# Optimization experiments

Measured on AMD Instinct MI355X. Metric: run time of the kernel, lower is better.

The kernel has to match this reference:

```python
import jax, jax.numpy as jnp
import numpy as np

B, T, C, V = 8, 2048, 1024, 32000


def setup_inputs() -> dict:
    key = jax.random.key(0)
    ks = jax.random.split(key, 12)
    s = 1.0 / np.sqrt(C)
    return {
        "input_tokens": jax.random.randint(ks[0], (B, T), 0, V),
        "xx_init": jnp.zeros((B, C), jnp.float32),
        "aa_init": jnp.zeros((B, C), jnp.float32),
        "bb_init": jnp.zeros((B, C), jnp.float32),
        "pp_init": jnp.zeros((B, C), jnp.float32),  # with aa=bb=0 this is equivalent to -inf init
        "emb": jax.random.normal(ks[1], (V, C), jnp.float32) * 0.02,
        "time_mix_k": jax.random.uniform(ks[2], (C,), jnp.float32),
        "time_mix_v": jax.random.uniform(ks[3], (C,), jnp.float32),
        "time_mix_r": jax.random.uniform(ks[4], (C,), jnp.float32),
        "time_decay": jax.random.normal(ks[5], (C,), jnp.float32) * 0.1,
        "time_first": jax.random.normal(ks[6], (C,), jnp.float32) * 0.1,
        "Wk": jax.random.normal(ks[7], (C, C), jnp.float32) * s,
        "Wv": jax.random.normal(ks[8], (C, C), jnp.float32) * s,
        "Wr": jax.random.normal(ks[9], (C, C), jnp.float32) * s,
        "Wo": jax.random.normal(ks[10], (C, C), jnp.float32) * s,
    }


def _wkv_scan(k, v, aa0, bb0, pp0, w, u):
    """Numerically-stable RWKV WKV recurrence.
    k, v: [T, B, C]; aa0/bb0/pp0: [B, C]; w (decay, negative), u (bonus): [C]."""
    def step(carry, kv):
        aa, bb, pp = carry
        kt, vt = kv
        ww = u + kt
        p = jnp.maximum(pp, ww)
        e1 = jnp.exp(pp - p)
        e2 = jnp.exp(ww - p)
        wkv = (e1 * aa + e2 * vt) / (e1 * bb + e2)
        ww2 = pp + w
        p2 = jnp.maximum(ww2, kt)
        e1b = jnp.exp(ww2 - p2)
        e2b = jnp.exp(kt - p2)
        return (e1b * aa + e2b * vt, e1b * bb + e2b, p2), wkv
    (aa, bb, pp), out = jax.lax.scan(step, (aa0, bb0, pp0), (k, v))
    return out, aa, bb, pp


def _forward(input_tokens, xx_init, aa_init, bb_init, pp_init, emb,
             time_mix_k, time_mix_v, time_mix_r, time_decay, time_first,
             Wk, Wv, Wr, Wo):
    x = emb[input_tokens]                                   # [B, T, C]
    xprev = jnp.concatenate([xx_init[:, None, :], x[:, :-1]], axis=1)  # token shift
    xk = x * time_mix_k + xprev * (1.0 - time_mix_k)
    xv = x * time_mix_v + xprev * (1.0 - time_mix_v)
    xr = x * time_mix_r + xprev * (1.0 - time_mix_r)
    k = jnp.einsum("btc,dc->btd", xk, Wk)
    v = jnp.einsum("btc,dc->btd", xv, Wv)
    r = jax.nn.sigmoid(jnp.einsum("btc,dc->btd", xr, Wr))
    w = -jnp.exp(time_decay)                                # per-channel decay
    u = time_first
    wkv, _, _, _ = _wkv_scan(jnp.swapaxes(k, 0, 1), jnp.swapaxes(v, 0, 1),
                             aa_init, bb_init, pp_init, w, u)
    wkv = jnp.swapaxes(wkv, 0, 1)                           # [B, T, C]
    rwkv = jnp.einsum("btc,dc->btd", r * wkv, Wo)
    e1 = rwkv[:, -1]          # final-step state
    e2 = rwkv.mean(axis=1)    # time-averaged state
    hx = (e1 + e2) * 0.5
    return jnp.stack([hx, hx])  # (hx, cx) stacked -> [2, B, C]


def reference(input_tokens, xx_init, aa_init, bb_init, pp_init, emb,
              time_mix_k, time_mix_v, time_mix_r, time_decay, time_first,
              Wk, Wv, Wr, Wo):
    return _forward(input_tokens, xx_init, aa_init, bb_init, pp_init, emb,
                    time_mix_k, time_mix_v, time_mix_r, time_decay, time_first,
                    Wk, Wv, Wr, Wo)
```

## Files before the change

### kernel.cpp

```cpp
#include <hip/hip_runtime.h>

#define Bdim 8
#define Tdim 2048
#define Cdim 1024
#define CHUNK 128
#define NCHUNK 16
#define BC (Bdim*Cdim)

typedef float floatx4 __attribute__((ext_vector_type(4)));
typedef _Float16 half8 __attribute__((ext_vector_type(8)));
typedef _Float16 half4v __attribute__((ext_vector_type(4)));

__device__ __forceinline__ void load16(const void* g, void* l) {
    __builtin_amdgcn_global_load_lds(
        (const __attribute__((address_space(1))) void*)g,
        (__attribute__((address_space(3))) void*)l, 16, 0, 0);
}

__global__ __launch_bounds__(256) void embed_mix(const int* __restrict__ tokens,
                                                 const float* __restrict__ xx_init,
                                                 const float* __restrict__ emb,
                                                 _Float16* __restrict__ xe) {
    int row = blockIdx.x;
    int b = row / (Tdim + 1);
    int tt = row % (Tdim + 1);
    const float* src;
    if (tt == 0) src = xx_init + (size_t)b * Cdim;
    else         src = emb + (size_t)tokens[b * Tdim + tt - 1] * Cdim;
    int c0 = threadIdx.x * 4;
    float4 f = *reinterpret_cast<const float4*>(src + c0);
    half4v h;
    h[0] = (_Float16)f.x; h[1] = (_Float16)f.y; h[2] = (_Float16)f.z; h[3] = (_Float16)f.w;
    *reinterpret_cast<half4v*>(xe + (size_t)row * Cdim + c0) = h;
}

__global__ __launch_bounds__(256) void mix3(const _Float16* __restrict__ xe,
                                            const float* __restrict__ tmk,
                                            const float* __restrict__ tmv,
                                            const float* __restrict__ tmr,
                                            _Float16* __restrict__ xk,
                                            _Float16* __restrict__ xv,
                                            _Float16* __restrict__ xr) {
    int row = blockIdx.x;
    int b = row >> 11;
    int t = row & (Tdim - 1);
    const _Float16* cur = xe + ((size_t)(b * (Tdim + 1) + t + 1)) * Cdim;
    const _Float16* prv = cur - Cdim;
    int c = threadIdx.x * 4;
    half4v cu = *reinterpret_cast<const half4v*>(cur + c);
    half4v pv = *reinterpret_cast<const half4v*>(prv + c);
    float4 mk = *reinterpret_cast<const float4*>(tmk + c);
    float4 mv = *reinterpret_cast<const float4*>(tmv + c);
    float4 mr = *reinterpret_cast<const float4*>(tmr + c);
    half4v hk, hv, hr;
    float cf[4] = {(float)cu[0], (float)cu[1], (float)cu[2], (float)cu[3]};
    float pf[4] = {(float)pv[0], (float)pv[1], (float)pv[2], (float)pv[3]};
    float mkf[4] = {mk.x, mk.y, mk.z, mk.w};
    float mvf[4] = {mv.x, mv.y, mv.z, mv.w};
    float mrf[4] = {mr.x, mr.y, mr.z, mr.w};
    #pragma unroll
    for (int j = 0; j < 4; j++) {
        hk[j] = (_Float16)(mkf[j] * cf[j] + (1.0f - mkf[j]) * pf[j]);
        hv[j] = (_Float16)(mvf[j] * cf[j] + (1.0f - mvf[j]) * pf[j]);
        hr[j] = (_Float16)(mrf[j] * cf[j] + (1.0f - mrf[j]) * pf[j]);
    }
    size_t o = (size_t)row * Cdim + c;
    *reinterpret_cast<half4v*>(xk + o) = hk;
    *reinterpret_cast<half4v*>(xv + o) = hv;
    *reinterpret_cast<half4v*>(xr + o) = hr;
}

__global__ __launch_bounds__(256) void wconv(const float* __restrict__ Wk,
                                             const float* __restrict__ Wv,
                                             const float* __restrict__ Wr,
                                             _Float16* __restrict__ Wh) {
    const float* W = blockIdx.y == 0 ? Wk : (blockIdx.y == 1 ? Wv : Wr);
    _Float16* dst = Wh + (size_t)blockIdx.y * Cdim * Cdim;
    int i = (blockIdx.x * 256 + threadIdx.x) * 4;
    float4 f = *reinterpret_cast<const float4*>(W + i);
    half4v h;
    h[0] = (_Float16)f.x; h[1] = (_Float16)f.y; h[2] = (_Float16)f.z; h[3] = (_Float16)f.w;
    *reinterpret_cast<half4v*>(dst + i) = h;
}

__global__ __launch_bounds__(512, 2) void gemm_kvr(const _Float16* __restrict__ xk,
                                                   const _Float16* __restrict__ xv,
                                                   const _Float16* __restrict__ xr,
                                                   const _Float16* __restrict__ Wh,
                                                   _Float16* __restrict__ ko,
                                                   _Float16* __restrict__ vo,
                                                   _Float16* __restrict__ ro) {
    const int which = blockIdx.y;
    const _Float16* X = which == 0 ? xk : (which == 1 ? xv : xr);
    const _Float16* W = Wh + (size_t)which * Cdim * Cdim;
    _Float16* out     = which == 0 ? ko : (which == 1 ? vo : ro);

    const int lin = blockIdx.x;
    const int xcd = lin & 7;
    const int loc = lin >> 3;
    const int mt = xcd * 8 + (loc >> 2);
    const int nt = loc & 3;
    const int m0 = mt * 256;
    const int n0 = nt * 256;

    __shared__ _Float16 As[4 * 8192];
    __shared__ _Float16 Bs[4 * 8192];

    const int tid = threadIdx.x;
    const int lane = tid & 63;
    const int wave = tid >> 6;
    const int wm = (wave >> 2) * 128;
    const int wn = (wave & 3) * 64;
    const int lr = lane & 15;
    const int lk = lane >> 4;
    const int sw = (lr >> 1) & 3;

    const _Float16* Asrc = X + (size_t)m0 * Cdim;
    const _Float16* Bsrc = W + (size_t)n0 * Cdim;

    floatx4 acc[8][4] = {};

    auto stage = [&](int kt) {
        const int p = kt & 3;
        const int k0 = kt * 32;
        #pragma unroll
        for (int i = 0; i < 2; i++) {
            int e = i * 512 + tid;
            int r = e >> 2;
            int cp = e & 3;
            int cl = cp ^ ((r >> 1) & 3);
            load16(Asrc + (size_t)r * Cdim + k0 + cl * 8, (char*)(As + p * 8192) + e * 16);
        }
        #pragma unroll
        for (int i = 0; i < 2; i++) {
            int e = i * 512 + tid;
            int r = e >> 2;
            int cp = e & 3;
            int cl = cp ^ ((r >> 1) & 3);
            load16(Bsrc + (size_t)r * Cdim + k0 + cl * 8, (char*)(Bs + p * 8192) + e * 16);
        }
    };

    auto compute = [&](int kt) {
        const int p = kt & 3;
        const _Float16* ap = As + p * 8192 + (wm + lr) * 32 + (lk ^ sw) * 8;
        const _Float16* bp = Bs + p * 8192 + (wn + lr) * 32 + (lk ^ sw) * 8;
        half8 af[8], bf[4];
        #pragma unroll
        for (int mi = 0; mi < 8; mi++)
            af[mi] = *reinterpret_cast<const half8*>(ap + mi * 16 * 32);
        #pragma unroll
        for (int ni = 0; ni < 4; ni++)
            bf[ni] = *reinterpret_cast<const half8*>(bp + ni * 16 * 32);
        __builtin_amdgcn_s_setprio(1);
        #pragma unroll
        for (int mi = 0; mi < 8; mi++)
            #pragma unroll
            for (int ni = 0; ni < 4; ni++)
                acc[mi][ni] = __builtin_amdgcn_mfma_f32_16x16x32_f16(af[mi], bf[ni], acc[mi][ni], 0, 0, 0);
        __builtin_amdgcn_s_setprio(0);
    };

    stage(0); stage(1); stage(2);
    asm volatile("s_waitcnt vmcnt(8)" ::: "memory");
    __builtin_amdgcn_s_barrier();

    for (int kt = 0; kt < 29; ++kt) {
        stage(kt + 3);
        compute(kt);
        asm volatile("s_waitcnt vmcnt(8)" ::: "memory");
        __builtin_amdgcn_s_barrier();
    }
    compute(29);
    asm volatile("s_waitcnt vmcnt(4)" ::: "memory");
    __builtin_amdgcn_s_barrier();
    compute(30);
    asm volatile("s_waitcnt vmcnt(0)" ::: "memory");
    __builtin_amdgcn_s_barrier();
    compute(31);

    #pragma unroll
    for (int mi = 0; mi < 8; mi++) {
        #pragma unroll
        for (int ni = 0; ni < 4; ni++) {
            #pragma unroll
            for (int reg = 0; reg < 4; reg++) {
                int mm = m0 + wm + mi * 16 + (lane >> 4) * 4 + reg;
                int nn = n0 + wn + ni * 16 + (lane & 15);
                float v = acc[mi][ni][reg];
                if (which == 2) v = 1.0f / (1.0f + __expf(-v));
                out[(size_t)mm * Cdim + nn] = (_Float16)v;
            }
        }
    }
}

__global__ __launch_bounds__(256) void scan_pass1(const _Float16* __restrict__ kb,
                                                  const _Float16* __restrict__ vb,
                                                  const float* __restrict__ tdecay,
                                                  float* __restrict__ tot_a,
                                                  float* __restrict__ tot_b,
                                                  float* __restrict__ tot_p) {
    int idx = blockIdx.x * 256 + threadIdx.x;
    int j = idx >> 13;
    int bc = idx & (BC - 1);
    int b = bc >> 10;
    int c = bc & (Cdim - 1);
    float w = -__expf(tdecay[c]);
    float aa = 0.0f, bb = 0.0f, pp = -1e30f;
    const _Float16* kp = kb + ((size_t)(b * Tdim + j * CHUNK)) * Cdim + c;
    const _Float16* vp = vb + ((size_t)(b * Tdim + j * CHUNK)) * Cdim + c;
    #pragma unroll 4
    for (int t = 0; t < CHUNK; t++) {
        float kt = (float)kp[(size_t)t * Cdim];
        float vt = (float)vp[(size_t)t * Cdim];
        float ww2 = pp + w;
        float p2 = fmaxf(ww2, kt);
        float e1 = __expf(ww2 - p2);
        float e2 = __expf(kt - p2);
        aa = e1 * aa + e2 * vt;
        bb = e1 * bb + e2;
        pp = p2;
    }
    tot_a[idx] = aa; tot_b[idx] = bb; tot_p[idx] = pp;
}

__global__ __launch_bounds__(256) void combine_chunks(const float* __restrict__ tot_a,
                                                      const float* __restrict__ tot_b,
                                                      const float* __restrict__ tot_p,
                                                      const float* __restrict__ aa_init,
                                                      const float* __restrict__ bb_init,
                                                      const float* __restrict__ pp_init,
                                                      const float* __restrict__ tdecay,
                                                      float* __restrict__ inc_a,
                                                      float* __restrict__ inc_b,
                                                      float* __restrict__ inc_p) {
    int idx = blockIdx.x * 256 + threadIdx.x;
    int c = idx & (Cdim - 1);
    float w = -__expf(tdecay[c]);
    float wL = w * (float)CHUNK;
    float a = aa_init[idx], b = bb_init[idx], p = pp_init[idx];
    for (int j = 0; j < NCHUNK; j++) {
        inc_a[j * BC + idx] = a;
        inc_b[j * BC + idx] = b;
        inc_p[j * BC + idx] = p;
        float ta = tot_a[j * BC + idx];
        float tb = tot_b[j * BC + idx];
        float tp = tot_p[j * BC + idx];
        float px = p + wL;
        float q = fmaxf(px, tp);
        float e1 = __expf(px - q);
        float e2 = __expf(tp - q);
        a = e1 * a + e2 * ta;
        b = e1 * b + e2 * tb;
        p = q;
    }
}

__global__ __launch_bounds__(256) void scan_pass2(const _Float16* __restrict__ kb,
                                                  const _Float16* __restrict__ vb,
                                                  const _Float16* __restrict__ rb,
                                                  const float* __restrict__ tdecay,
                                                  const float* __restrict__ tfirst,
                                                  const float* __restrict__ inc_a,
                                                  const float* __restrict__ inc_b,
                                                  const float* __restrict__ inc_p,
                                                  float* __restrict__ partial,
                                                  float* __restrict__ ylast) {
    int idx = blockIdx.x * 256 + threadIdx.x;
    int j = idx >> 13;
    int bc = idx & (BC - 1);
    int b = bc >> 10;
    int c = bc & (Cdim - 1);
    float w = -__expf(tdecay[c]);
    float u = tfirst[c];
    float aa = inc_a[idx], bb = inc_b[idx], pp = inc_p[idx];
    const size_t base = ((size_t)(b * Tdim + j * CHUNK)) * Cdim + c;
    const _Float16* kp = kb + base;
    const _Float16* vp = vb + base;
    const _Float16* rp = rb + base;
    float sum = 0.0f, ylv = 0.0f;
    #pragma unroll 4
    for (int t = 0; t < CHUNK; t++) {
        float kt = (float)kp[(size_t)t * Cdim];
        float vt = (float)vp[(size_t)t * Cdim];
        float rt = (float)rp[(size_t)t * Cdim];
        float ww = u + kt;
        float p = fmaxf(pp, ww);
        float e1 = __expf(pp - p);
        float e2 = __expf(ww - p);
        float wkv = (e1 * aa + e2 * vt) / (e1 * bb + e2);
        float y = rt * wkv;
        sum += y;
        ylv = y;
        float ww2 = pp + w;
        float p2 = fmaxf(ww2, kt);
        float e1b = __expf(ww2 - p2);
        float e2b = __expf(kt - p2);
        aa = e1b * aa + e2b * vt;
        bb = e1b * bb + e2b;
        pp = p2;
    }
    partial[idx] = sum;
    if (j == NCHUNK - 1) ylast[bc] = ylv;
}

__global__ __launch_bounds__(256) void reduce_z(const float* __restrict__ partial,
                                                const float* __restrict__ ylast,
                                                float* __restrict__ z) {
    int idx = blockIdx.x * 256 + threadIdx.x;
    float s = 0.0f;
    for (int j = 0; j < NCHUNK; j++) s += partial[j * BC + idx];
    z[idx] = 0.5f * (ylast[idx] + s * (1.0f / (float)Tdim));
}

__global__ __launch_bounds__(256) void final_out(const float* __restrict__ z,
                                                 const float* __restrict__ Wo,
                                                 float* __restrict__ out) {
    int gw = (blockIdx.x * 256 + threadIdx.x) >> 6;
    int lane = threadIdx.x & 63;
    int b = gw >> 10;
    int d = gw & (Cdim - 1);
    const float* zr = z + (size_t)b * Cdim;
    const float* wr = Wo + (size_t)d * Cdim;
    float acc = 0.0f;
    #pragma unroll
    for (int i = lane; i < Cdim; i += 64) acc += zr[i] * wr[i];
    #pragma unroll
    for (int off = 32; off > 0; off >>= 1) acc += __shfl_down(acc, off);
    if (lane == 0) {
        out[(size_t)b * Cdim + d] = acc;
        out[(size_t)BC + (size_t)b * Cdim + d] = acc;
    }
}

extern "C" void kernel_launch(void* const* d_in, const int* in_sizes, int n_in,
                              void* d_out, int out_size, void* d_ws, size_t ws_size,
                              hipStream_t stream) {
    const int*   tokens  = (const int*)d_in[0];
    const float* xx_init = (const float*)d_in[1];
    const float* aa_init = (const float*)d_in[2];
    const float* bb_init = (const float*)d_in[3];
    const float* pp_init = (const float*)d_in[4];
    const float* emb     = (const float*)d_in[5];
    const float* tmk     = (const float*)d_in[6];
    const float* tmv     = (const float*)d_in[7];
    const float* tmr     = (const float*)d_in[8];
    const float* tdecay  = (const float*)d_in[9];
    const float* tfirst  = (const float*)d_in[10];
    const float* Wk      = (const float*)d_in[11];
    const float* Wv      = (const float*)d_in[12];
    const float* Wr      = (const float*)d_in[13];
    const float* Wo      = (const float*)d_in[14];
    float* out = (float*)d_out;

    char* ws = (char*)d_ws;
    size_t off = 0;
    auto alloc = [&](size_t bytes) -> void* {
        void* p = ws + off;
        off += (bytes + 255) & ~(size_t)255;
        return p;
    };
    _Float16* xe = (_Float16*)alloc((size_t)Bdim * (Tdim + 1) * Cdim * 2);
    _Float16* xkb = (_Float16*)alloc((size_t)Bdim * Tdim * Cdim * 2);
    _Float16* xvb = (_Float16*)alloc((size_t)Bdim * Tdim * Cdim * 2);
    _Float16* xrb = (_Float16*)alloc((size_t)Bdim * Tdim * Cdim * 2);
    _Float16* kb = xe;
    _Float16* vb = (_Float16*)alloc((size_t)Bdim * Tdim * Cdim * 2);
    _Float16* rb = (_Float16*)alloc((size_t)Bdim * Tdim * Cdim * 2);
    _Float16* Wh = (_Float16*)alloc((size_t)3 * Cdim * Cdim * 2);
    float* tot_a = (float*)alloc((size_t)NCHUNK * BC * 4);
    float* tot_b = (float*)alloc((size_t)NCHUNK * BC * 4);
    float* tot_p = (float*)alloc((size_t)NCHUNK * BC * 4);
    float* inc_a = (float*)alloc((size_t)NCHUNK * BC * 4);
    float* inc_b = (float*)alloc((size_t)NCHUNK * BC * 4);
    float* inc_p = (float*)alloc((size_t)NCHUNK * BC * 4);
    float* partial = (float*)alloc((size_t)NCHUNK * BC * 4);
    float* ylast   = (float*)alloc((size_t)BC * 4);
    float* zbuf    = (float*)alloc((size_t)BC * 4);

    embed_mix<<<Bdim * (Tdim + 1), 256, 0, stream>>>(tokens, xx_init, emb, xe);
    mix3<<<Bdim * Tdim, 256, 0, stream>>>(xe, tmk, tmv, tmr, xkb, xvb, xrb);
    wconv<<<dim3(1024, 3), 256, 0, stream>>>(Wk, Wv, Wr, Wh);
    gemm_kvr<<<dim3(256, 3), 512, 0, stream>>>(xkb, xvb, xrb, Wh, kb, vb, rb);
    scan_pass1<<<(NCHUNK * BC) / 256, 256, 0, stream>>>(kb, vb, tdecay, tot_a, tot_b, tot_p);
    combine_chunks<<<BC / 256, 256, 0, stream>>>(tot_a, tot_b, tot_p, aa_init, bb_init, pp_init,
                                                 tdecay, inc_a, inc_b, inc_p);
    scan_pass2<<<(NCHUNK * BC) / 256, 256, 0, stream>>>(kb, vb, rb, tdecay, tfirst,
                                                        inc_a, inc_b, inc_p, partial, ylast);
    reduce_z<<<BC / 256, 256, 0, stream>>>(partial, ylast, zbuf);
    final_out<<<(BC / 4), 256, 0, stream>>>(zbuf, Wo, out);
}
```

Before: 410.6 us.

## Split GEMM k-tile into two MFMA phases interleaved with A/B LDS staging

Each k-tile of the fp16 MFMA GEMM now runs in two halves. The first loads half of the A fragments plus all B fragments, issues the A prefetch for tile kt+3, and runs 16 MFMAs. The second loads the remaining A fragments, issues the B prefetch, and runs the other 16 MFMAs. This spreads global->LDS traffic across the compute and interleaves LDS reads with MFMA in a ping-pong style schedule. The cost is extra workgroup barriers and sched_barriers per k-tile, which may stall waves.

```diff
diff --git a/kernel.cpp b/kernel.cpp
--- a/kernel.cpp
+++ b/kernel.cpp
@@ -120,7 +120,7 @@
 
     floatx4 acc[8][4] = {};
 
-    auto stage = [&](int kt) {
+    auto stageA = [&](int kt) {
         const int p = kt & 3;
         const int k0 = kt * 32;
         #pragma unroll
@@ -131,6 +131,10 @@
             int cl = cp ^ ((r >> 1) & 3);
             load16(Asrc + (size_t)r * Cdim + k0 + cl * 8, (char*)(As + p * 8192) + e * 16);
         }
+    };
+    auto stageB = [&](int kt) {
+        const int p = kt & 3;
+        const int k0 = kt * 32;
         #pragma unroll
         for (int i = 0; i < 2; i++) {
             int e = i * 512 + tid;
@@ -141,43 +145,63 @@
         }
     };
 
-    auto compute = [&](int kt) {
+    auto ktile = [&](int kt, bool st) {
         const int p = kt & 3;
         const _Float16* ap = As + p * 8192 + (wm + lr) * 32 + (lk ^ sw) * 8;
         const _Float16* bp = Bs + p * 8192 + (wn + lr) * 32 + (lk ^ sw) * 8;
         half8 af[8], bf[4];
         #pragma unroll
-        for (int mi = 0; mi < 8; mi++)
-            af[mi] = *reinterpret_cast<const half8*>(ap + mi * 16 * 32);
+        for (int mi = 0; mi < 4; mi++)
+            af[mi] = *reinterpret_cast<const half8*>(ap + mi * 512);
         #pragma unroll
         for (int ni = 0; ni < 4; ni++)
-            bf[ni] = *reinterpret_cast<const half8*>(bp + ni * 16 * 32);
+            bf[ni] = *reinterpret_cast<const half8*>(bp + ni * 512);
+        if (st) stageA(kt + 3);
+        __builtin_amdgcn_s_barrier();
+        asm volatile("s_waitcnt lgkmcnt(0)" ::: "memory");
+        __builtin_amdgcn_sched_barrier(0);
         __builtin_amdgcn_s_setprio(1);
         #pragma unroll
-        for (int mi = 0; mi < 8; mi++)
+        for (int mi = 0; mi < 4; mi++)
             #pragma unroll
             for (int ni = 0; ni < 4; ni++)
                 acc[mi][ni] = __builtin_amdgcn_mfma_f32_16x16x32_f16(af[mi], bf[ni], acc[mi][ni], 0, 0, 0);
         __builtin_amdgcn_s_setprio(0);
+        __builtin_amdgcn_sched_barrier(0);
+        __builtin_amdgcn_s_barrier();
+        #pragma unroll
+        for (int mi = 4; mi < 8; mi++)
+            af[mi] = *reinterpret_cast<const half8*>(ap + mi * 512);
+        if (st) stageB(kt + 3);
+        __builtin_amdgcn_s_barrier();
+        asm volatile("s_waitcnt lgkmcnt(0)" ::: "memory");
+        __builtin_amdgcn_sched_barrier(0);
+        __builtin_amdgcn_s_setprio(1);
+        #pragma unroll
+        for (int mi = 4; mi < 8; mi++)
+            #pragma unroll
+            for (int ni = 0; ni < 4; ni++)
+                acc[mi][ni] = __builtin_amdgcn_mfma_f32_16x16x32_f16(af[mi], bf[ni], acc[mi][ni], 0, 0, 0);
+        __builtin_amdgcn_s_setprio(0);
+        __builtin_amdgcn_sched_barrier(0);
     };
 
-    stage(0); stage(1); stage(2);
+    stageA(0); stageB(0); stageA(1); stageB(1); stageA(2); stageB(2);
     asm volatile("s_waitcnt vmcnt(8)" ::: "memory");
     __builtin_amdgcn_s_barrier();
 
     for (int kt = 0; kt < 29; ++kt) {
-        stage(kt + 3);
-        compute(kt);
+        ktile(kt, true);
         asm volatile("s_waitcnt vmcnt(8)" ::: "memory");
         __builtin_amdgcn_s_barrier();
     }
-    compute(29);
+    ktile(29, false);
     asm volatile("s_waitcnt vmcnt(4)" ::: "memory");
     __builtin_amdgcn_s_barrier();
-    compute(30);
+    ktile(30, false);
     asm volatile("s_waitcnt vmcnt(0)" ::: "memory");
     __builtin_amdgcn_s_barrier();
-    compute(31);
+    ktile(31, false);
 
     #pragma unroll
     for (int mi = 0; mi < 8; mi++) {
```

After: 410.3 us. No clear change (-0.1%).
